# Optimization experiments

Hardware: AMD Instinct MI355X
Metric: run time of the kernel (lower is better)

Reference implementation:

```python
import jax, jax.numpy as jnp
import numpy as np

N_QUBITS = 4
N_LAYERS = 2
BATCH = 1048576


def setup_inputs() -> dict:
    key = jax.random.key(0)
    k1, k2 = jax.random.split(key)
    noise = jax.random.normal(k1, (BATCH, N_QUBITS), dtype=jnp.float32)
    weights = jax.random.normal(k2, (N_LAYERS, N_QUBITS), dtype=jnp.float32)
    return {"noise": noise, "weights": weights}


def _apply_1q(state, U, wire):
    # state: (B, 2,2,2,2) complex; U: (2,2) or (B,2,2)
    s = jnp.moveaxis(state, wire + 1, -1)
    if U.ndim == 3:
        s = jnp.einsum('bij,b...j->b...i', U, s)
    else:
        s = jnp.einsum('ij,...j->...i', U, s)
    return jnp.moveaxis(s, -1, wire + 1)


def _apply_cnot(state, ctrl, tgt):
    ca, ta = ctrl + 1, tgt + 1
    s0 = jnp.take(state, 0, axis=ca)
    s1 = jnp.take(state, 1, axis=ca)
    ta_shift = ta if ta < ca else ta - 1  # target axis after removing ctrl axis
    s1 = jnp.flip(s1, axis=ta_shift)      # X on target when ctrl=1
    return jnp.stack([s0, s1], axis=ca)


def reference(noise, weights):
    B = noise.shape[0]
    # |0...0> initial state, shape (B, 2,2,2,2)
    state = jnp.zeros((B,) + (2,) * N_QUBITS, dtype=jnp.complex64)
    state = state.at[(slice(None),) + (0,) * N_QUBITS].set(1.0)

    # RX(noise[w]) on each wire (batched angles)
    for w in range(N_QUBITS):
        th = noise[:, w] * 0.5
        c, s = jnp.cos(th), jnp.sin(th)
        U = jnp.stack([jnp.stack([c + 0j, -1j * s], -1),
                       jnp.stack([-1j * s, c + 0j], -1)], -2).astype(jnp.complex64)
        state = _apply_1q(state, U, w)

    for layer in range(N_LAYERS):
        for w in range(N_QUBITS):
            state = _apply_cnot(state, w, (w + 1) % N_QUBITS)
        for w in range(N_QUBITS):
            th = weights[layer, w] * 0.5
            c, s = jnp.cos(th), jnp.sin(th)
            U = jnp.stack([jnp.stack([c, -s]), jnp.stack([s, c])]).astype(jnp.complex64)
            state = _apply_1q(state, U, w)

    probs = (state.real ** 2 + state.imag ** 2).astype(jnp.float32)
    cols = []
    for w in range(N_QUBITS):
        sum_axes = tuple(a for a in range(1, N_QUBITS + 1) if a != w + 1)
        marg = probs.sum(axis=sum_axes)  # (B, 2)
        # <Z> = p0 - p1, output = (<Z>+1)/2 = p0
        cols.append(marg[:, 0])
    return jnp.stack(cols, axis=-1)
```

## Files before the change

### kernel.cpp

```cpp
#include <hip/hip_runtime.h>
#include <math.h>


__global__ void trig_kernel(const float* __restrict__ w, float* __restrict__ trig) {
    int i = threadIdx.x;
    if (i < 8) {
        float th = w[i] * 0.5f;
        trig[i]     = cosf(th);
        trig[i + 8] = sinf(th);
    }
}

#define CNOT(cb, tb)                                                  \
    {                                                                 \
        _Pragma("unroll") for (int i = 0; i < 16; i++)                \
            if ((i & (cb)) && !(i & (tb))) {                          \
                int j = i | (tb);                                     \
                float t;                                              \
                t = re[i]; re[i] = re[j]; re[j] = t;                  \
                t = im[i]; im[i] = im[j]; im[j] = t;                  \
            }                                                         \
    }

#define RY(bit, cc, ss)                                               \
    {                                                                 \
        _Pragma("unroll") for (int i = 0; i < 16; i++)                \
            if (!(i & (bit))) {                                       \
                int j = i | (bit);                                    \
                float r0 = re[i], r1 = re[j];                         \
                float i0 = im[i], i1 = im[j];                         \
                re[i] = (cc) * r0 - (ss) * r1;                        \
                re[j] = (ss) * r0 + (cc) * r1;                        \
                im[i] = (cc) * i0 - (ss) * i1;                        \
                im[j] = (ss) * i0 + (cc) * i1;                        \
            }                                                         \
    }

__global__ __launch_bounds__(256) void qc_kernel(const float* __restrict__ noise,
                                                 const float* __restrict__ trig,
                                                 float* __restrict__ out, int B) {
    int b = blockIdx.x * blockDim.x + threadIdx.x;
    if (b >= B) return;

    float4 nv = reinterpret_cast<const float4*>(noise)[b];
    float c0, s0, c1, s1, c2, s2, c3, s3;
    __sincosf(nv.x * 0.5f, &s0, &c0);
    __sincosf(nv.y * 0.5f, &s1, &c1);
    __sincosf(nv.z * 0.5f, &s2, &c2);
    __sincosf(nv.w * 0.5f, &s3, &c3);

    float wc[8], wsn[8];
#pragma unroll
    for (int i = 0; i < 8; i++) {
        wc[i]  = trig[i];
        wsn[i] = trig[i + 8];
    }

    float m01[4], m23[4];
    m01[0] = c0 * c1; m01[1] = c0 * s1; m01[2] = s0 * c1; m01[3] = s0 * s1;
    m23[0] = c2 * c3; m23[1] = c2 * s3; m23[2] = s2 * c3; m23[3] = s2 * s3;

    float re[16], im[16];
#pragma unroll
    for (int i = 0; i < 16; i++) {
        float m = m01[i >> 2] * m23[i & 3];
        int pc = __popc(i) & 3;
        re[i] = (pc == 0) ? m : (pc == 2) ? -m : 0.0f;
        im[i] = (pc == 1) ? -m : (pc == 3) ? m : 0.0f;
    }

#pragma unroll
    for (int layer = 0; layer < 2; layer++) {
        CNOT(8, 4);
        CNOT(4, 2);
        CNOT(2, 1);
        CNOT(1, 8);
        RY(8, wc[layer * 4 + 0], wsn[layer * 4 + 0]);
        RY(4, wc[layer * 4 + 1], wsn[layer * 4 + 1]);
        RY(2, wc[layer * 4 + 2], wsn[layer * 4 + 2]);
        RY(1, wc[layer * 4 + 3], wsn[layer * 4 + 3]);
    }

    float p[16];
#pragma unroll
    for (int i = 0; i < 16; i++) p[i] = re[i] * re[i] + im[i] * im[i];

    float o0 = 0.f, o1 = 0.f, o2 = 0.f, o3 = 0.f;
#pragma unroll
    for (int i = 0; i < 16; i++) {
        if (!(i & 8)) o0 += p[i];
        if (!(i & 4)) o1 += p[i];
        if (!(i & 2)) o2 += p[i];
        if (!(i & 1)) o3 += p[i];
    }
    reinterpret_cast<float4*>(out)[b] = make_float4(o0, o1, o2, o3);
}

extern "C" void kernel_launch(void* const* d_in, const int* in_sizes, int n_in,
                              void* d_out, int out_size, void* d_ws, size_t ws_size,
                              hipStream_t stream) {
    const float* noise   = (const float*)d_in[0];
    const float* weights = (const float*)d_in[1];
    float* trig = (float*)d_ws;
    float* out  = (float*)d_out;
    int B = in_sizes[0] / 4;

    trig_kernel<<<1, 64, 0, stream>>>(weights, trig);
    qc_kernel<<<(B + 255) / 256, 256, 0, stream>>>(noise, trig, out, B);
}
```

Measured before the change: 79.84 us.

## Fuse weight trig into main kernel, use FMAs and shared partial sums for marginals

Removes the separate trig kernel launch by computing the layer weight cos/sin inline in each thread with __sincosf. This drops one launch and the dependency between the two kernels, at the cost of a few extra sincos per thread and lower-precision intrinsics for the weight angles. The rotation and probability arithmetic now uses explicit FMAs. The marginal sums reuse shared partial sums (row and column groups) instead of four independent accumulations.

```diff
diff --git a/kernel.cpp b/kernel.cpp
--- a/kernel.cpp
+++ b/kernel.cpp
@@ -1,15 +1,6 @@
 #include <hip/hip_runtime.h>
 #include <math.h>
 
-
-__global__ void trig_kernel(const float* __restrict__ w, float* __restrict__ trig) {
-    int i = threadIdx.x;
-    if (i < 8) {
-        float th = w[i] * 0.5f;
-        trig[i]     = cosf(th);
-        trig[i + 8] = sinf(th);
-    }
-}
 
 #define CNOT(cb, tb)                                                  \
     {                                                                 \
@@ -29,18 +20,25 @@
                 int j = i | (bit);                                    \
                 float r0 = re[i], r1 = re[j];                         \
                 float i0 = im[i], i1 = im[j];                         \
-                re[i] = (cc) * r0 - (ss) * r1;                        \
-                re[j] = (ss) * r0 + (cc) * r1;                        \
-                im[i] = (cc) * i0 - (ss) * i1;                        \
-                im[j] = (ss) * i0 + (cc) * i1;                        \
+                re[i] = __builtin_fmaf((cc), r0, -((ss) * r1));       \
+                re[j] = __builtin_fmaf((ss), r0, (cc) * r1);          \
+                im[i] = __builtin_fmaf((cc), i0, -((ss) * i1));       \
+                im[j] = __builtin_fmaf((ss), i0, (cc) * i1);          \
             }                                                         \
     }
 
 __global__ __launch_bounds__(256) void qc_kernel(const float* __restrict__ noise,
-                                                 const float* __restrict__ trig,
+                                                 const float* __restrict__ weights,
                                                  float* __restrict__ out, int B) {
     int b = blockIdx.x * blockDim.x + threadIdx.x;
     if (b >= B) return;
+
+    float wc[8], wsn[8];
+#pragma unroll
+    for (int i = 0; i < 8; i++) {
+        float th = weights[i] * 0.5f;
+        __sincosf(th, &wsn[i], &wc[i]);
+    }
 
     float4 nv = reinterpret_cast<const float4*>(noise)[b];
     float c0, s0, c1, s1, c2, s2, c3, s3;
@@ -48,13 +46,6 @@
     __sincosf(nv.y * 0.5f, &s1, &c1);
     __sincosf(nv.z * 0.5f, &s2, &c2);
     __sincosf(nv.w * 0.5f, &s3, &c3);
-
-    float wc[8], wsn[8];
-#pragma unroll
-    for (int i = 0; i < 8; i++) {
-        wc[i]  = trig[i];
-        wsn[i] = trig[i + 8];
-    }
 
     float m01[4], m23[4];
     m01[0] = c0 * c1; m01[1] = c0 * s1; m01[2] = s0 * c1; m01[3] = s0 * s1;
@@ -83,16 +74,20 @@
 
     float p[16];
 #pragma unroll
-    for (int i = 0; i < 16; i++) p[i] = re[i] * re[i] + im[i] * im[i];
+    for (int i = 0; i < 16; i++) p[i] = __builtin_fmaf(im[i], im[i], re[i] * re[i]);
 
-    float o0 = 0.f, o1 = 0.f, o2 = 0.f, o3 = 0.f;
+    float g[4], h[4];
 #pragma unroll
-    for (int i = 0; i < 16; i++) {
-        if (!(i & 8)) o0 += p[i];
-        if (!(i & 4)) o1 += p[i];
-        if (!(i & 2)) o2 += p[i];
-        if (!(i & 1)) o3 += p[i];
-    }
+    for (int x = 0; x < 4; x++)
+        g[x] = ((p[4 * x + 0] + p[4 * x + 1]) + (p[4 * x + 2] + p[4 * x + 3]));
+#pragma unroll
+    for (int y = 0; y < 4; y++)
+        h[y] = ((p[y] + p[y + 4]) + (p[y + 8] + p[y + 12]));
+
+    float o0 = g[0] + g[1];
+    float o1 = g[0] + g[2];
+    float o2 = h[0] + h[1];
+    float o3 = h[0] + h[2];
     reinterpret_cast<float4*>(out)[b] = make_float4(o0, o1, o2, o3);
 }
 
@@ -101,10 +96,8 @@
                               hipStream_t stream) {
     const float* noise   = (const float*)d_in[0];
     const float* weights = (const float*)d_in[1];
-    float* trig = (float*)d_ws;
-    float* out  = (float*)d_out;
+    float* out = (float*)d_out;
     int B = in_sizes[0] / 4;
 
-    trig_kernel<<<1, 64, 0, stream>>>(weights, trig);
-    qc_kernel<<<(B + 255) / 256, 256, 0, stream>>>(noise, trig, out, B);
+    qc_kernel<<<(B + 255) / 256, 256, 0, stream>>>(noise, weights, out, B);
 }
```

Result: no change. 79.88 us (+0.1%).
